# Performance work log

Hardware: AMD Instinct MI355X
Metric: run time of the kernel (lower is better)

## Reference

```python
import jax, jax.numpy as jnp
import numpy as np
from jax import lax

B, N, L, P, C, D = 64, 20000, 336, 96, 16, 64
COARSE_K, TOPM, ALPHA, TEMP = 80, 20, 0.7, 0.1
CAT_DIM, N_TAB, GH = 16, 17, 128
ID_MIN = np.array([0,0,0,0,0,1,1,0,0,0,0,0,0,0,0,0,0], dtype=np.int64)
ID_MAX = np.array([2047,255,4095,23,6,12,53,3,1,1,15,7,2,2,2,2,1], dtype=np.int64)

def _gelu(x):
    return jax.nn.gelu(x, approximate=False)

def _mlp2(x, w1, b1, w2, b2):
    return _gelu(x @ w1 + b1) @ w2 + b2

def _ln(x, g, b):
    m = x.mean(-1, keepdims=True)
    v = jnp.var(x, axis=-1, keepdims=True)
    return (x - m) / jnp.sqrt(v + 1e-5) * g + b

def _unit(x):
    return x / (jnp.linalg.norm(x, axis=-1, keepdims=True) + 1e-12)

def setup_inputs():
    key = jax.random.key(0)
    ks = jax.random.split(key, 24)
    s = 0.02
    z = jnp.zeros
    return {
        'meta_ids': jax.random.randint(ks[0], (B, N_TAB), 0, 2),
        'exogenous_vars': jax.random.normal(ks[1], (B, 8)),
        'local_state_by_period': jax.random.normal(ks[2], (B, 3, 4)),
        'x': jax.random.normal(ks[3], (B, L, C)),
        'pool_context': jax.random.normal(ks[4], (N, D)),
        'pool_x': jax.random.normal(ks[5], (N, L, C)),
        'pool_y': jax.random.normal(ks[6], (N, P, C)),
        'emb_tables': jax.random.normal(ks[7], (N_TAB, 4096, CAT_DIM)) * s,
        'cat_w1': jax.random.normal(ks[8], (N_TAB * CAT_DIM, D)) * s, 'cat_b1': z((D,)),
        'cat_w2': jax.random.normal(ks[9], (D, D)) * s, 'cat_b2': z((D,)),
        'exo_w1': jax.random.normal(ks[10], (8, D)) * s, 'exo_b1': z((D,)),
        'exo_w2': jax.random.normal(ks[11], (D, D)) * s, 'exo_b2': z((D,)),
        'loc_w1': jax.random.normal(ks[12], (4, D)) * s, 'loc_b1': z((D,)),
        'loc_w2': jax.random.normal(ks[13], (D, D)) * s, 'loc_b2': z((D,)),
        'ln_g': jnp.ones((D,)), 'ln_b': z((D,)),
        'gate_w1': jax.random.normal(ks[14], (2 * D + 2, GH)) * s, 'gate_b1': z((GH,)),
        'gate_w2': jax.random.normal(ks[15], (GH, 1)) * s, 'gate_b2': z((1,)),
    }

def _forward(meta_ids, exogenous_vars, local_state_by_period, x, pool_context, pool_x, pool_y,
             emb_tables, cat_w1, cat_b1, cat_w2, cat_b2, exo_w1, exo_b1, exo_w2, exo_b2,
             loc_w1, loc_b1, loc_w2, loc_b2, ln_g, ln_b, gate_w1, gate_b1, gate_w2, gate_b2):
    # --- hierarchical context encoder ---
    ids = jnp.clip(meta_ids, jnp.asarray(ID_MIN)[None, :], jnp.asarray(ID_MAX)[None, :])
    # per-table embedding lookup -> [B, 17, cat_dim]
    cat = jax.vmap(lambda t, i: t[i], in_axes=(0, 1), out_axes=1)(emb_tables, ids)
    cat = cat.reshape(B, N_TAB * CAT_DIM)
    cat_ctx = _mlp2(cat, cat_w1, cat_b1, cat_w2, cat_b2)
    cat_ctx = cat_ctx + _mlp2(exogenous_vars, exo_w1, exo_b1, exo_w2, exo_b2)
    loc = _mlp2(local_state_by_period.reshape(-1, 4), loc_w1, loc_b1, loc_w2, loc_b2).reshape(B, 3, D)
    ctx = _ln(cat_ctx[:, None, :] + loc, ln_g, ln_b)       # [B, 3, D]
    q = ctx.mean(axis=1)                                    # pooled query context [B, D]
    # --- coarse retrieval: cosine sim over meta pool ---
    meta_sim = _unit(q) @ _unit(pool_context).T             # [B, N]
    meta_c, coarse_idx = lax.top_k(meta_sim, COARSE_K)      # [B, K]
    cand_ctx = pool_context[coarse_idx]                     # [B, K, D]
    cand_x = pool_x[coarse_idx]                             # [B, K, L, C]
    # --- fine similarity on raw series ---
    xf = _unit(x.reshape(B, L * C))
    cf = _unit(cand_x.reshape(B, COARSE_K, L * C))
    series_sim = jnp.einsum('bd,bkd->bk', xf, cf)
    combined = ALPHA * meta_c + (1.0 - ALPHA) * series_sim
    comb_m, li = lax.top_k(combined, TOPM)                  # [B, M]
    meta_m = jnp.take_along_axis(meta_c, li, axis=1)
    ctx_m = jnp.take_along_axis(cand_ctx, li[..., None], axis=1)   # [B, M, D]
    fin_idx = jnp.take_along_axis(coarse_idx, li, axis=1)
    cand_y = pool_y[fin_idx]                                # [B, M, P, C]
    # --- gated aggregation ---
    gate_in = jnp.concatenate([
        jnp.broadcast_to(q[:, None, :], (B, TOPM, D)), ctx_m,
        comb_m[..., None], meta_m[..., None]], axis=-1)     # [B, M, 2D+2]
    gate = _mlp2(gate_in, gate_w1, gate_b1, gate_w2, gate_b2)[..., 0]
    w = jax.nn.softmax(comb_m / TEMP + gate, axis=-1)       # [B, M]
    return jnp.einsum('bm,bmpc->bpc', w, cand_y)            # [B, P, C]

def reference(meta_ids, exogenous_vars, local_state_by_period, x, pool_context, pool_x, pool_y,
              emb_tables, cat_w1, cat_b1, cat_w2, cat_b2, exo_w1, exo_b1, exo_w2, exo_b2,
              loc_w1, loc_b1, loc_w2, loc_b2, ln_g, ln_b, gate_w1, gate_b1, gate_w2, gate_b2):
    return _forward(meta_ids, exogenous_vars, local_state_by_period, x, pool_context, pool_x, pool_y,
                    emb_tables, cat_w1, cat_b1, cat_w2, cat_b2, exo_w1, exo_b1, exo_w2, exo_b2,
                    loc_w1, loc_b1, loc_w2, loc_b2, ln_g, ln_b, gate_w1, gate_b1, gate_w2, gate_b2)
```

## Files before the change

kernel.cpp:

```cpp
#include <hip/hip_runtime.h>
#include <math.h>

typedef unsigned int u32;

#define BB 64
#define NN 20000
#define LL 336
#define PP 96
#define CC 16
#define DD 64
#define KC 80
#define TM 20
#define LC 5376
#define NTAB 17
#define GH 128
#define CAP 2048

__constant__ int c_idmin[17] = {0,0,0,0,0,1,1,0,0,0,0,0,0,0,0,0,0};
__constant__ int c_idmax[17] = {2047,255,4095,23,6,12,53,3,1,1,15,7,2,2,2,2,1};

__device__ __forceinline__ float gelu(float x){ return 0.5f*x*(1.0f + erff(x*0.70710678118654752440f)); }
__device__ __forceinline__ float wred(float v){
  #pragma unroll
  for(int m=32;m>=1;m>>=1) v += __shfl_xor(v, m, 64);
  return v;
}
__device__ __forceinline__ u32 fkey(float f){
  u32 u = __float_as_uint(f);
  return (u & 0x80000000u) ? ~u : (u | 0x80000000u);
}

#define OFF_Q     0u
#define OFF_QN    16384u
#define OFF_XN    32768u
#define OFF_CIDX  33024u
#define OFF_METC  53504u
#define OFF_COMB  73984u
#define OFF_FIDX  94464u
#define OFF_W     99584u
#define OFF_SIM   106496u

__global__ __launch_bounds__(64) void k_ctx(
    const int* __restrict__ mids, const float* __restrict__ exo,
    const float* __restrict__ locs, const float* __restrict__ x,
    const float* __restrict__ emb,
    const float* __restrict__ cw1, const float* __restrict__ cb1,
    const float* __restrict__ cw2, const float* __restrict__ cb2,
    const float* __restrict__ ew1, const float* __restrict__ eb1,
    const float* __restrict__ ew2, const float* __restrict__ eb2,
    const float* __restrict__ lw1, const float* __restrict__ lb1,
    const float* __restrict__ lw2, const float* __restrict__ lb2,
    const float* __restrict__ lng, const float* __restrict__ lnb,
    float* __restrict__ q, float* __restrict__ qn, float* __restrict__ xn)
{
  int b = blockIdx.x, j = threadIdx.x;
  __shared__ float s_cat[272];
  __shared__ float s_h[64];
  __shared__ float s_exo[8];
  __shared__ float s_loc[12];

  for(int e=j; e<272; e+=64){
    int t=e>>4, c=e&15;
    int id = mids[b*NTAB + t];
    if(id < c_idmin[t]) id = c_idmin[t];
    if(id > c_idmax[t]) id = c_idmax[t];
    s_cat[e] = emb[((size_t)t*4096 + id)*16 + c];
  }
  if(j<8)  s_exo[j] = exo[b*8+j];
  if(j<12) s_loc[j] = locs[b*12+j];
  __syncthreads();

  float a = cb1[j];
  for(int i=0;i<272;i++) a += s_cat[i]*cw1[i*64+j];
  s_h[j] = gelu(a);
  __syncthreads();
  float cc = cb2[j];
  for(int k=0;k<64;k++) cc += s_h[k]*cw2[k*64+j];
  __syncthreads();

  a = eb1[j];
  for(int i=0;i<8;i++) a += s_exo[i]*ew1[i*64+j];
  s_h[j] = gelu(a);
  __syncthreads();
  float ec = eb2[j];
  for(int k=0;k<64;k++) ec += s_h[k]*ew2[k*64+j];
  cc += ec;
  __syncthreads();

  float lr[3];
  for(int r=0;r<3;r++){
    a = lb1[j];
    for(int i=0;i<4;i++) a += s_loc[r*4+i]*lw1[i*64+j];
    s_h[j] = gelu(a);
    __syncthreads();
    float o = lb2[j];
    for(int k=0;k<64;k++) o += s_h[k]*lw2[k*64+j];
    lr[r] = o;
    __syncthreads();
  }

  float g = lng[j], be = lnb[j];
  float qa = 0.f;
  for(int r=0;r<3;r++){
    float v = cc + lr[r];
    float mean = wred(v) * (1.0f/64.0f);
    float d = v - mean;
    float var = wred(d*d) * (1.0f/64.0f);
    qa += d / sqrtf(var + 1e-5f) * g + be;
  }
  float qv = qa * (1.0f/3.0f);
  q[b*64+j] = qv;
  float s2 = wred(qv*qv);
  qn[b*64+j] = qv / (sqrtf(s2) + 1e-12f);

  float xa = 0.f;
  for(int e=j; e<LC; e+=64){ float f = x[(size_t)b*LC+e]; xa += f*f; }
  xa = wred(xa);
  if(j==0) xn[b] = sqrtf(xa);
}

__device__ __attribute__((noinline)) float row_sim(const float* pr, const float* sq)
{
  const float4* p4 = (const float4*)pr;
  float dot=0.f, ns=0.f;
  #pragma unroll
  for(int i=0;i<16;i++){
    float4 u = p4[i];
    dot += u.x*sq[i*4+0] + u.y*sq[i*4+1] + u.z*sq[i*4+2] + u.w*sq[i*4+3];
    ns  += u.x*u.x + u.y*u.y + u.z*u.z + u.w*u.w;
  }
  return dot / (sqrtf(ns) + 1e-12f);
}

__global__ __launch_bounds__(256) void k_sim(const float* __restrict__ pc,
    const float* __restrict__ qn, float* __restrict__ sim)
{
  __shared__ float s_pc[64*68];
  __shared__ float s_qn[4*64];
  int n0 = blockIdx.x << 6;
  int b0 = blockIdx.y << 2;
  int tid = threadIdx.x;

  const float4* pc4 = (const float4*)pc;
  for(int e=tid; e<64*16; e+=256){
    int r = e>>4, c = e&15;
    float4 v;
    if(n0 + r < NN) v = pc4[(size_t)(n0+r)*16 + c];
    else            v = make_float4(0.f,0.f,0.f,0.f);
    *(float4*)&s_pc[r*68 + c*4] = v;
  }
  s_qn[tid] = qn[(size_t)(b0 + (tid>>6))*64 + (tid&63)];
  __syncthreads();

  int bl = tid>>6, ln = tid&63;
  const float4* q4 = (const float4*)&s_qn[bl*64];
  const float4* p4 = (const float4*)&s_pc[ln*68];
  float dot=0.f, ns=0.f;
  #pragma unroll
  for(int i=0;i<16;i++){
    float4 p = p4[i], qv = q4[i];
    dot += p.x*qv.x + p.y*qv.y + p.z*qv.z + p.w*qv.w;
    ns  += p.x*p.x + p.y*p.y + p.z*p.z + p.w*p.w;
  }
  int n = n0 + ln;
  if(n < NN) sim[(size_t)(b0+bl)*NN + n] = dot / (sqrtf(ns) + 1e-12f);
}

__global__ __launch_bounds__(256) void k_sel(const float* __restrict__ sim,
    int* __restrict__ cidx_out, float* __restrict__ metc)
{
  __shared__ u32 hist[4096];
  __shared__ u32 cs[256];
  __shared__ float cval[CAP];
  __shared__ int  cidxs[CAP];
  __shared__ int s_T; __shared__ u32 s_above;
  __shared__ int s_T2; __shared__ u32 s_above2;
  __shared__ u32 s_na, s_nc, s_nb;
  __shared__ float swv[4]; __shared__ int swi[4];
  int b = blockIdx.x, tid = threadIdx.x;
  const float* srow = sim + (size_t)b*NN;
  const float4* srow4 = (const float4*)srow;

  for(int e=tid;e<4096;e+=256) hist[e]=0;
  if(tid==0){ s_na=0; s_nc=0; s_nb=0; }
  for(int e=tid;e<KC;e+=256){ cidx_out[b*KC+e]=0; metc[b*KC+e]=-1.0f; }
  __syncthreads();

  for(int i=tid;i<NN/4;i+=256){
    float4 v = srow4[i];
    atomicAdd(&hist[fkey(v.x)>>20], 1u);
    atomicAdd(&hist[fkey(v.y)>>20], 1u);
    atomicAdd(&hist[fkey(v.z)>>20], 1u);
    atomicAdd(&hist[fkey(v.w)>>20], 1u);
  }
  __syncthreads();
  u32 c=0;
  #pragma unroll
  for(int i=0;i<16;i++) c += hist[tid*16+i];
  cs[tid]=c;
  __syncthreads();
  if(tid==0){
    u32 acc=0, above=0; int T=0;
    for(int ch=255; ch>=0; --ch){
      if(acc + cs[ch] >= (u32)KC){
        for(int bin=ch*16+15;; --bin){
          if(acc + hist[bin] >= (u32)KC){ T=bin; above=acc; break; }
          acc += hist[bin];
        }
        break;
      }
      acc += cs[ch];
    }
    s_T = T; s_above = above;
  }
  __syncthreads();
  int T = s_T; u32 above = s_above;

  for(int i=tid;i<NN/4;i+=256){
    float4 vv = srow4[i];
    float va[4] = {vv.x, vv.y, vv.z, vv.w};
    #pragma unroll
    for(int cix=0;cix<4;cix++){
      float v = va[cix];
      int k = (int)(fkey(v)>>20);
      if(k > T){
        u32 p = atomicAdd(&s_na,1u);
        if(p < (u32)KC){ int n = i*4+cix; cidx_out[b*KC+p] = n; metc[b*KC+p] = v; }
      } else if(k == T){
        u32 p = atomicAdd(&s_nc,1u);
        if(p < CAP){ cval[p]=v; cidxs[p]=i*4+cix; }
      }
    }
  }
  __syncthreads();
  int need = KC - (int)above; if(need < 0) need = 0;
  int Mc = (int)s_nc; if(Mc > CAP) Mc = CAP;

  for(int e=tid;e<4096;e+=256) hist[e]=0;
  __syncthreads();
  for(int e=tid;e<Mc;e+=256) atomicAdd(&hist[(fkey(cval[e])>>8)&0xFFFu], 1u);
  __syncthreads();
  u32 c2=0;
  #pragma unroll
  for(int i=0;i<16;i++) c2 += hist[tid*16+i];
  cs[tid]=c2;
  __syncthreads();
  if(tid==0){
    if(need == 0){ s_T2 = 4096; s_above2 = 0; }
    else {
      u32 acc=0, above2=0; int T2=0;
      for(int ch=255; ch>=0; --ch){
        if(acc + cs[ch] >= (u32)need){
          for(int bin=ch*16+15;; --bin){
            if(acc + hist[bin] >= (u32)need){ T2=bin; above2=acc; break; }
            acc += hist[bin];
          }
          break;
        }
        acc += cs[ch];
      }
      s_T2 = T2; s_above2 = above2;
    }
  }
  __syncthreads();
  int T2 = s_T2; u32 above2 = s_above2;

  for(int e=tid;e<Mc;e+=256){
    float v = cval[e];
    int sub = (int)((fkey(v)>>8)&0xFFFu);
    if(sub > T2){
      u32 p = atomicAdd(&s_nb,1u);
      if(p < (u32)need){
        cidx_out[b*KC+above+p] = cidxs[e];
        metc[b*KC+above+p] = v;
      }
      cval[e] = -3.0e38f;
    }
  }
  __syncthreads();

  int need2 = need - (int)above2; if(need2 < 0) need2 = 0;
  for(int r=0;r<need2;r++){
    float v=-3.0e38f; int i=-1;
    for(int e=tid;e<Mc;e+=256){ if(cval[e]>v){v=cval[e];i=e;} }
    int lane=tid&63, w=tid>>6;
    #pragma unroll
    for(int m=32;m>=1;m>>=1){
      float ov=__shfl_xor(v,m,64); int oi=__shfl_xor(i,m,64);
      if(ov>v){v=ov;i=oi;}
    }
    if(lane==0){ swv[w]=v; swi[w]=i; }
    __syncthreads();
    if(tid==0){
      float bv=swv[0]; int bi=swi[0];
      for(int k2=1;k2<4;k2++) if(swv[k2]>bv){bv=swv[k2];bi=swi[k2];}
      if(bi >= 0){
        cidx_out[b*KC+above+above2+r] = cidxs[bi];
        metc[b*KC+above+above2+r] = bv;
        cval[bi] = -3.0e38f;
      }
    }
    __syncthreads();
  }
}

__global__ __launch_bounds__(256) void k_csel(const float* __restrict__ pc,
    const float* __restrict__ qn, int* __restrict__ cidx_out, float* __restrict__ metc)
{
  __shared__ u32 hist[4096];
  __shared__ u32 cs[256];
  __shared__ float cval[CAP];
  __shared__ int  cidxs[CAP];
  __shared__ float s_qn[64];
  __shared__ int s_T; __shared__ u32 s_above;
  __shared__ u32 s_na, s_nc;
  __shared__ float swv[4]; __shared__ int swi[4];
  int b = blockIdx.x, tid = threadIdx.x;

  for(int e=tid;e<4096;e+=256) hist[e]=0;
  if(tid<64) s_qn[tid] = qn[b*64+tid];
  if(tid==0){ s_na=0; s_nc=0; }
  for(int e=tid;e<KC;e+=256){ cidx_out[b*KC+e]=0; metc[b*KC+e]=-1.0f; }
  __syncthreads();

  for(int n=tid;n<NN;n+=256){
    float v = row_sim(pc + (size_t)n*64, s_qn);
    atomicAdd(&hist[fkey(v)>>20], 1u);
  }
  __syncthreads();
  u32 c=0;
  #pragma unroll
  for(int i=0;i<16;i++) c += hist[tid*16+i];
  cs[tid]=c;
  __syncthreads();
  if(tid==0){
    u32 acc=0, above=0; int T=0;
    for(int ch=255; ch>=0; --ch){
      if(acc + cs[ch] >= (u32)KC){
        for(int bin=ch*16+15;; --bin){
          if(acc + hist[bin] >= (u32)KC){ T=bin; above=acc; break; }
          acc += hist[bin];
        }
        break;
      }
      acc += cs[ch];
    }
    s_T = T; s_above = above;
  }
  __syncthreads();
  int T = s_T; u32 above = s_above;

  for(int n=tid;n<NN;n+=256){
    float v = row_sim(pc + (size_t)n*64, s_qn);
    int k = (int)(fkey(v)>>20);
    if(k > T){
      u32 p = atomicAdd(&s_na,1u);
      if(p < (u32)KC){ cidx_out[b*KC+p] = n; metc[b*KC+p] = v; }
    } else if(k == T){
      u32 p = atomicAdd(&s_nc,1u);
      if(p < CAP){ cval[p]=v; cidxs[p]=n; }
    }
  }
  __syncthreads();
  int need = KC - (int)above; if(need < 0) need = 0;
  int Mc = (int)s_nc; if(Mc > CAP) Mc = CAP;
  for(int r=0;r<need;r++){
    float v=-3.0e38f; int i=-1;
    for(int e=tid;e<Mc;e+=256){ if(cval[e]>v){v=cval[e];i=e;} }
    int lane=tid&63, w=tid>>6;
    #pragma unroll
    for(int m=32;m>=1;m>>=1){
      float ov=__shfl_xor(v,m,64); int oi=__shfl_xor(i,m,64);
      if(ov>v){v=ov;i=oi;}
    }
    if(lane==0){ swv[w]=v; swi[w]=i; }
    __syncthreads();
    if(tid==0){
      float bv=swv[0]; int bi=swi[0];
      for(int k2=1;k2<4;k2++) if(swv[k2]>bv){bv=swv[k2];bi=swi[k2];}
      if(bi >= 0){
        cidx_out[b*KC+above+r] = cidxs[bi];
        metc[b*KC+above+r] = bv;
        cval[bi] = -3.0e38f;
      }
    }
    __syncthreads();
  }
}

__global__ __launch_bounds__(256) void k_fine(const float* __restrict__ px,
    const float* __restrict__ x, const int* __restrict__ cidx,
    const float* __restrict__ metc, const float* __restrict__ xn,
    float* __restrict__ comb)
{
  __shared__ float s_red[8];
  int blk = blockIdx.x;
  int b = blk / KC, k = blk % KC;
  int idx = cidx[b*KC+k];
  if(idx < 0) idx = 0;
  if(idx >= NN) idx = NN-1;
  const float4* pr = (const float4*)(px + (size_t)idx*LC);
  const float4* xr = (const float4*)(x + (size_t)b*LC);
  int tid = threadIdx.x;
  float dot=0.f, ns=0.f;
  for(int i=tid; i<LC/4; i+=256){
    float4 a = pr[i], cx = xr[i];
    dot += cx.x*a.x + cx.y*a.y + cx.z*a.z + cx.w*a.w;
    ns  += a.x*a.x + a.y*a.y + a.z*a.z + a.w*a.w;
  }
  dot = wred(dot); ns = wred(ns);
  int lane=tid&63, w=tid>>6;
  if(lane==0){ s_red[w]=dot; s_red[4+w]=ns; }
  __syncthreads();
  if(tid==0){
    float dd = s_red[0]+s_red[1]+s_red[2]+s_red[3];
    float nn = s_red[4]+s_red[5]+s_red[6]+s_red[7];
    float s = dd / ((xn[b]+1e-12f)*(sqrtf(nn)+1e-12f));
    comb[b*KC+k] = 0.7f*metc[b*KC+k] + (1.0f-0.7f)*s;
  }
}

__global__ __launch_bounds__(256) void k_gate(const float* __restrict__ comb,
    const float* __restrict__ metc, const int* __restrict__ cidx,
    const float* __restrict__ q, const float* __restrict__ pc,
    const float* __restrict__ gw1, const float* __restrict__ gb1,
    const float* __restrict__ gw2, const float* __restrict__ gb2,
    int* __restrict__ fidx, float* __restrict__ wout)
{
  __shared__ float s_w1[130*128];
  __shared__ float s_comb[80], s_met[80]; __shared__ int s_ci[80];
  __shared__ float s_q[64];
  __shared__ float s_ctxw[4*64];
  __shared__ float selv[20], selm[20]; __shared__ int seli[20];
  __shared__ float s_gate[20];
  __shared__ float swv2[4]; __shared__ int swi2[4];
  int b=blockIdx.x, tid=threadIdx.x;

  const float4* g4 = (const float4*)gw1;
  float4* s4 = (float4*)s_w1;
  for(int e=tid;e<4160;e+=256) s4[e] = g4[e];
  if(tid<80){
    s_comb[tid]=comb[b*KC+tid]; s_met[tid]=metc[b*KC+tid];
    int ci = cidx[b*KC+tid];
    if(ci<0) ci=0;
    if(ci>=NN) ci=NN-1;
    s_ci[tid]=ci;
  }
  if(tid<64) s_q[tid]=q[b*64+tid];
  __syncthreads();

  for(int r=0;r<TM;r++){
    float v=-3.0e38f; int i=-1;
    if(tid<80){ v=s_comb[tid]; i=tid; }
    int lane=tid&63, w=tid>>6;
    #pragma unroll
    for(int m=32;m>=1;m>>=1){
      float ov=__shfl_xor(v,m,64); int oi=__shfl_xor(i,m,64);
      if(ov>v){v=ov;i=oi;}
    }
    if(lane==0){ swv2[w]=v; swi2[w]=i; }
    __syncthreads();
    if(tid==0){
      float bv=swv2[0]; int bi=swi2[0];
      for(int k2=1;k2<4;k2++) if(swv2[k2]>bv){bv=swv2[k2];bi=swi2[k2];}
      if(bi<0) bi=0;
      selv[r]=bv; selm[r]=s_met[bi]; seli[r]=s_ci[bi];
      s_comb[bi]=-3.0e38f;
    }
    __syncthreads();
  }

  int w = tid>>6, ln = tid&63;
  for(int m=w; m<TM; m+=4){
    s_ctxw[w*64+ln] = pc[(size_t)seli[m]*64 + ln];
    float a  = gb1[ln];
    float a2 = gb1[64+ln];
    for(int i=0;i<64;i++){
      float qi = s_q[i];
      a  += qi*s_w1[i*128+ln];
      a2 += qi*s_w1[i*128+64+ln];
    }
    for(int i=0;i<64;i++){
      float ci = s_ctxw[w*64+i];
      a  += ci*s_w1[(64+i)*128+ln];
      a2 += ci*s_w1[(64+i)*128+64+ln];
    }
    a  += selv[m]*s_w1[128*128+ln];
    a  += selm[m]*s_w1[129*128+ln];
    a2 += selv[m]*s_w1[128*128+64+ln];
    a2 += selm[m]*s_w1[129*128+64+ln];
    float h = gelu(a)*gw2[ln] + gelu(a2)*gw2[64+ln];
    float s = wred(h);
    if(ln==0) s_gate[m] = s + gb2[0];
  }
  __syncthreads();

  if(tid==0){
    float lg[20]; float mx=-3.0e38f;
    for(int m=0;m<TM;m++){ lg[m] = selv[m]*10.0f + s_gate[m]; if(lg[m]>mx) mx=lg[m]; }
    float ss=0.f;
    for(int m=0;m<TM;m++){ lg[m]=expf(lg[m]-mx); ss+=lg[m]; }
    for(int m=0;m<TM;m++){ wout[b*TM+m]=lg[m]/ss; fidx[b*TM+m]=seli[m]; }
  }
}

__global__ __launch_bounds__(192) void k_out(const float* __restrict__ py,
    const int* __restrict__ fidx, const float* __restrict__ wv,
    float* __restrict__ out)
{
  __shared__ float s_w[20]; __shared__ int s_i[20];
  int b=blockIdx.x, half=blockIdx.y, tid=threadIdx.x;
  if(tid<TM){
    s_w[tid]=wv[b*TM+tid];
    int ii=fidx[b*TM+tid];
    if(ii<0) ii=0;
    if(ii>=NN) ii=NN-1;
    s_i[tid]=ii;
  }
  __syncthreads();
  int e4 = half*192 + tid;
  const float4* py4 = (const float4*)py;
  float4 acc = make_float4(0.f,0.f,0.f,0.f);
  #pragma unroll
  for(int m=0;m<TM;m++){
    float4 v = py4[(size_t)s_i[m]*(PP*CC/4) + e4];
    float wm = s_w[m];
    acc.x += wm*v.x; acc.y += wm*v.y; acc.z += wm*v.z; acc.w += wm*v.w;
  }
  ((float4*)out)[(size_t)b*(PP*CC/4) + e4] = acc;
}

extern "C" void kernel_launch(void* const* d_in, const int* in_sizes, int n_in,
                              void* d_out, int out_size, void* d_ws, size_t ws_size,
                              hipStream_t stream) {
  const int*   mids = (const int*)d_in[0];
  const float* exo  = (const float*)d_in[1];
  const float* locs = (const float*)d_in[2];
  const float* x    = (const float*)d_in[3];
  const float* pc   = (const float*)d_in[4];
  const float* px   = (const float*)d_in[5];
  const float* py   = (const float*)d_in[6];
  const float* emb  = (const float*)d_in[7];
  const float* cw1  = (const float*)d_in[8];
  const float* cb1  = (const float*)d_in[9];
  const float* cw2  = (const float*)d_in[10];
  const float* cb2  = (const float*)d_in[11];
  const float* ew1  = (const float*)d_in[12];
  const float* eb1  = (const float*)d_in[13];
  const float* ew2  = (const float*)d_in[14];
  const float* eb2  = (const float*)d_in[15];
  const float* lw1  = (const float*)d_in[16];
  const float* lb1  = (const float*)d_in[17];
  const float* lw2  = (const float*)d_in[18];
  const float* lb2  = (const float*)d_in[19];
  const float* lng  = (const float*)d_in[20];
  const float* lnb  = (const float*)d_in[21];
  const float* gw1  = (const float*)d_in[22];
  const float* gb1  = (const float*)d_in[23];
  const float* gw2  = (const float*)d_in[24];
  const float* gb2  = (const float*)d_in[25];
  float* out = (float*)d_out;

  char* ws = (char*)d_ws;
  float* q    = (float*)(ws + OFF_Q);
  float* qn   = (float*)(ws + OFF_QN);
  float* xn   = (float*)(ws + OFF_XN);
  int*   cidx = (int*)  (ws + OFF_CIDX);
  float* metc = (float*)(ws + OFF_METC);
  float* comb = (float*)(ws + OFF_COMB);
  int*   fidx = (int*)  (ws + OFF_FIDX);
  float* wv   = (float*)(ws + OFF_W);
  float* sims = (float*)(ws + OFF_SIM);

  k_ctx<<<BB, 64, 0, stream>>>(mids, exo, locs, x, emb,
      cw1, cb1, cw2, cb2, ew1, eb1, ew2, eb2,
      lw1, lb1, lw2, lb2, lng, lnb, q, qn, xn);

  size_t need_sim = (size_t)OFF_SIM + (size_t)BB*NN*sizeof(float);
  if(ws_size >= need_sim){
    k_sim<<<dim3((NN+63)/64, BB/4), 256, 0, stream>>>(pc, qn, sims);
    k_sel<<<BB, 256, 0, stream>>>(sims, cidx, metc);
  } else {
    k_csel<<<BB, 256, 0, stream>>>(pc, qn, cidx, metc);
  }

  k_fine<<<BB*KC, 256, 0, stream>>>(px, x, cidx, metc, xn, comb);
  k_gate<<<BB, 256, 0, stream>>>(comb, metc, cidx, q, pc,
      gw1, gb1, gw2, gb2, fidx, wv);
  k_out<<<dim3(BB,2), 192, 0, stream>>>(py, fidx, wv, out);
}
```

Before: 754.9 us.

## Build coarse histogram inside similarity kernel and fuse gating with output gather

The similarity kernel now handles all 64 queries per pool tile, keeping each pool row in registers and computing its norm once. It also builds the 4096-bin per-query radix histogram in global memory, using wave-aggregated atomics. The histogram buffer is zeroed inside the context kernel, and the selection kernel loads the precomputed histogram instead of rescanning the similarity rows. The gating and output-gather kernels are merged, so one launch and a small workspace round trip go away. In exchange, k_sim issues global atomics and launches far fewer blocks, and the output gather runs on only 64 blocks.

```diff
diff --git a/kernel.cpp b/kernel.cpp
--- a/kernel.cpp
+++ b/kernel.cpp
@@ -36,9 +36,10 @@
 #define OFF_CIDX  33024u
 #define OFF_METC  53504u
 #define OFF_COMB  73984u
-#define OFF_FIDX  94464u
-#define OFF_W     99584u
 #define OFF_SIM   106496u
+#define OFF_HIST  5226496u
+#define WS_NEED   6275072u
+#define GHIST_U4  65536
 
 __global__ __launch_bounds__(64) void k_ctx(
     const int* __restrict__ mids, const float* __restrict__ exo,
@@ -51,13 +52,20 @@
     const float* __restrict__ lw1, const float* __restrict__ lb1,
     const float* __restrict__ lw2, const float* __restrict__ lb2,
     const float* __restrict__ lng, const float* __restrict__ lnb,
-    float* __restrict__ q, float* __restrict__ qn, float* __restrict__ xn)
+    float* __restrict__ q, float* __restrict__ qn, float* __restrict__ xn,
+    u32* __restrict__ ghist)
 {
   int b = blockIdx.x, j = threadIdx.x;
   __shared__ float s_cat[272];
   __shared__ float s_h[64];
   __shared__ float s_exo[8];
   __shared__ float s_loc[12];
+
+  if(ghist){
+    uint4* g4 = (uint4*)ghist;
+    int gid = b*64 + j;
+    for(int e=gid; e<GHIST_U4; e+=4096) g4[e] = make_uint4(0u,0u,0u,0u);
+  }
 
   for(int e=j; e<272; e+=64){
     int t=e>>4, c=e&15;
@@ -133,12 +141,11 @@
 }
 
 __global__ __launch_bounds__(256) void k_sim(const float* __restrict__ pc,
-    const float* __restrict__ qn, float* __restrict__ sim)
+    const float* __restrict__ qn, float* __restrict__ sim, u32* __restrict__ ghist)
 {
   __shared__ float s_pc[64*68];
-  __shared__ float s_qn[4*64];
+  __shared__ float s_qn[64*64];
   int n0 = blockIdx.x << 6;
-  int b0 = blockIdx.y << 2;
   int tid = threadIdx.x;
 
   const float4* pc4 = (const float4*)pc;
@@ -149,25 +156,48 @@
     else            v = make_float4(0.f,0.f,0.f,0.f);
     *(float4*)&s_pc[r*68 + c*4] = v;
   }
-  s_qn[tid] = qn[(size_t)(b0 + (tid>>6))*64 + (tid&63)];
-  __syncthreads();
-
-  int bl = tid>>6, ln = tid&63;
-  const float4* q4 = (const float4*)&s_qn[bl*64];
-  const float4* p4 = (const float4*)&s_pc[ln*68];
-  float dot=0.f, ns=0.f;
+  const float4* qn4 = (const float4*)qn;
+  for(int e=tid; e<1024; e+=256) ((float4*)s_qn)[e] = qn4[e];
+  __syncthreads();
+
+  int w = tid>>6, ln = tid&63;
+  int n = n0 + ln;
+  bool valid = (n < NN);
+
+  float4 pr[16];
   #pragma unroll
-  for(int i=0;i<16;i++){
-    float4 p = p4[i], qv = q4[i];
-    dot += p.x*qv.x + p.y*qv.y + p.z*qv.z + p.w*qv.w;
-    ns  += p.x*p.x + p.y*p.y + p.z*p.z + p.w*p.w;
-  }
-  int n = n0 + ln;
-  if(n < NN) sim[(size_t)(b0+bl)*NN + n] = dot / (sqrtf(ns) + 1e-12f);
+  for(int i=0;i<16;i++) pr[i] = *(const float4*)&s_pc[ln*68 + i*4];
+  float ns = 0.f;
+  #pragma unroll
+  for(int i=0;i<16;i++) ns += pr[i].x*pr[i].x + pr[i].y*pr[i].y + pr[i].z*pr[i].z + pr[i].w*pr[i].w;
+  float denom = sqrtf(ns) + 1e-12f;
+
+  unsigned long long vmask = __ballot(valid);
+  for(int bi=w; bi<64; bi+=4){
+    const float4* q4 = (const float4*)&s_qn[bi*64];
+    float dot = 0.f;
+    #pragma unroll
+    for(int i=0;i<16;i++){
+      float4 qv = q4[i];
+      dot += pr[i].x*qv.x + pr[i].y*qv.y + pr[i].z*qv.z + pr[i].w*qv.w;
+    }
+    float v = dot / denom;
+    if(valid) sim[(size_t)bi*NN + n] = v;
+
+    u32 key = fkey(v)>>20;
+    unsigned long long active = vmask;
+    while(active){
+      int leader = __ffsll((long long)active) - 1;
+      u32 lk = __shfl(key, leader, 64);
+      unsigned long long eq = __ballot(valid && key==lk);
+      if(ln==leader) atomicAdd(&ghist[bi*4096+lk], (u32)__popcll(eq));
+      active &= ~eq;
+    }
+  }
 }
 
 __global__ __launch_bounds__(256) void k_sel(const float* __restrict__ sim,
-    int* __restrict__ cidx_out, float* __restrict__ metc)
+    const u32* __restrict__ ghist, int* __restrict__ cidx_out, float* __restrict__ metc)
 {
   __shared__ u32 hist[4096];
   __shared__ u32 cs[256];
@@ -181,19 +211,11 @@
   const float* srow = sim + (size_t)b*NN;
   const float4* srow4 = (const float4*)srow;
 
-  for(int e=tid;e<4096;e+=256) hist[e]=0;
+  for(int e=tid;e<4096;e+=256) hist[e] = ghist[b*4096+e];
   if(tid==0){ s_na=0; s_nc=0; s_nb=0; }
   for(int e=tid;e<KC;e+=256){ cidx_out[b*KC+e]=0; metc[b*KC+e]=-1.0f; }
   __syncthreads();
 
-  for(int i=tid;i<NN/4;i+=256){
-    float4 v = srow4[i];
-    atomicAdd(&hist[fkey(v.x)>>20], 1u);
-    atomicAdd(&hist[fkey(v.y)>>20], 1u);
-    atomicAdd(&hist[fkey(v.z)>>20], 1u);
-    atomicAdd(&hist[fkey(v.w)>>20], 1u);
-  }
-  __syncthreads();
   u32 c=0;
   #pragma unroll
   for(int i=0;i<16;i++) c += hist[tid*16+i];
@@ -420,12 +442,12 @@
   }
 }
 
-__global__ __launch_bounds__(256) void k_gate(const float* __restrict__ comb,
+__global__ __launch_bounds__(256) void k_gateout(const float* __restrict__ comb,
     const float* __restrict__ metc, const int* __restrict__ cidx,
     const float* __restrict__ q, const float* __restrict__ pc,
     const float* __restrict__ gw1, const float* __restrict__ gb1,
     const float* __restrict__ gw2, const float* __restrict__ gb2,
-    int* __restrict__ fidx, float* __restrict__ wout)
+    const float* __restrict__ py, float* __restrict__ out)
 {
   __shared__ float s_w1[130*128];
   __shared__ float s_comb[80], s_met[80]; __shared__ int s_ci[80];
@@ -433,6 +455,7 @@
   __shared__ float s_ctxw[4*64];
   __shared__ float selv[20], selm[20]; __shared__ int seli[20];
   __shared__ float s_gate[20];
+  __shared__ float s_wf[20];
   __shared__ float swv2[4]; __shared__ int swi2[4];
   int b=blockIdx.x, tid=threadIdx.x;
 
@@ -500,34 +523,21 @@
     for(int m=0;m<TM;m++){ lg[m] = selv[m]*10.0f + s_gate[m]; if(lg[m]>mx) mx=lg[m]; }
     float ss=0.f;
     for(int m=0;m<TM;m++){ lg[m]=expf(lg[m]-mx); ss+=lg[m]; }
-    for(int m=0;m<TM;m++){ wout[b*TM+m]=lg[m]/ss; fidx[b*TM+m]=seli[m]; }
-  }
-}
-
-__global__ __launch_bounds__(192) void k_out(const float* __restrict__ py,
-    const int* __restrict__ fidx, const float* __restrict__ wv,
-    float* __restrict__ out)
-{
-  __shared__ float s_w[20]; __shared__ int s_i[20];
-  int b=blockIdx.x, half=blockIdx.y, tid=threadIdx.x;
-  if(tid<TM){
-    s_w[tid]=wv[b*TM+tid];
-    int ii=fidx[b*TM+tid];
-    if(ii<0) ii=0;
-    if(ii>=NN) ii=NN-1;
-    s_i[tid]=ii;
-  }
-  __syncthreads();
-  int e4 = half*192 + tid;
+    for(int m=0;m<TM;m++) s_wf[m]=lg[m]/ss;
+  }
+  __syncthreads();
+
   const float4* py4 = (const float4*)py;
-  float4 acc = make_float4(0.f,0.f,0.f,0.f);
-  #pragma unroll
-  for(int m=0;m<TM;m++){
-    float4 v = py4[(size_t)s_i[m]*(PP*CC/4) + e4];
-    float wm = s_w[m];
-    acc.x += wm*v.x; acc.y += wm*v.y; acc.z += wm*v.z; acc.w += wm*v.w;
-  }
-  ((float4*)out)[(size_t)b*(PP*CC/4) + e4] = acc;
+  for(int e4=tid; e4<PP*CC/4; e4+=256){
+    float4 acc = make_float4(0.f,0.f,0.f,0.f);
+    #pragma unroll
+    for(int m=0;m<TM;m++){
+      float4 v = py4[(size_t)seli[m]*(PP*CC/4) + e4];
+      float wm = s_wf[m];
+      acc.x += wm*v.x; acc.y += wm*v.y; acc.z += wm*v.z; acc.w += wm*v.w;
+    }
+    ((float4*)out)[(size_t)b*(PP*CC/4) + e4] = acc;
+  }
 }
 
 extern "C" void kernel_launch(void* const* d_in, const int* in_sizes, int n_in,
@@ -568,24 +578,24 @@
   int*   cidx = (int*)  (ws + OFF_CIDX);
   float* metc = (float*)(ws + OFF_METC);
   float* comb = (float*)(ws + OFF_COMB);
-  int*   fidx = (int*)  (ws + OFF_FIDX);
-  float* wv   = (float*)(ws + OFF_W);
   float* sims = (float*)(ws + OFF_SIM);
+  u32*   ghist= (u32*)  (ws + OFF_HIST);
+
+  bool big = (ws_size >= (size_t)WS_NEED);
 
   k_ctx<<<BB, 64, 0, stream>>>(mids, exo, locs, x, emb,
       cw1, cb1, cw2, cb2, ew1, eb1, ew2, eb2,
-      lw1, lb1, lw2, lb2, lng, lnb, q, qn, xn);
-
-  size_t need_sim = (size_t)OFF_SIM + (size_t)BB*NN*sizeof(float);
-  if(ws_size >= need_sim){
-    k_sim<<<dim3((NN+63)/64, BB/4), 256, 0, stream>>>(pc, qn, sims);
-    k_sel<<<BB, 256, 0, stream>>>(sims, cidx, metc);
+      lw1, lb1, lw2, lb2, lng, lnb, q, qn, xn,
+      big ? ghist : (u32*)nullptr);
+
+  if(big){
+    k_sim<<<(NN+63)/64, 256, 0, stream>>>(pc, qn, sims, ghist);
+    k_sel<<<BB, 256, 0, stream>>>(sims, ghist, cidx, metc);
   } else {
     k_csel<<<BB, 256, 0, stream>>>(pc, qn, cidx, metc);
   }
 
   k_fine<<<BB*KC, 256, 0, stream>>>(px, x, cidx, metc, xn, comb);
-  k_gate<<<BB, 256, 0, stream>>>(comb, metc, cidx, q, pc,
-      gw1, gb1, gw2, gb2, fidx, wv);
-  k_out<<<dim3(BB,2), 192, 0, stream>>>(py, fidx, wv, out);
-}
+  k_gateout<<<BB, 256, 0, stream>>>(comb, metc, cidx, q, pc,
+      gw1, gb1, gw2, gb2, py, out);
+}
```

Result: slower. 899.9 us (+19.2%).
